# Kernel tuning notes

Measured on AMD Instinct MI355X. Metric: run time of the kernel, lower is better.

Reference implementation:

```python
import jax, jax.numpy as jnp
import numpy as np
from jax import lax

EPS = 1e-12

def _l2norm(v, axis):
    n = jnp.linalg.norm(v, axis=axis, keepdims=True)
    return v / jnp.maximum(n, EPS)

def setup_inputs() -> dict:
    key = jax.random.key(0)
    k1, k2, k3 = jax.random.split(key, 3)
    C, H, W, K = 512, 192, 192, 64
    x = jax.random.normal(k1, (C, H, W), dtype=jnp.float32)
    conv_w = jax.random.normal(k2, (K, C), dtype=jnp.float32) * 0.05  # 1x1 conv, no bias (vladv2=False)
    centroids = jax.random.uniform(k3, (K, C), dtype=jnp.float32)
    return {"x": x, "conv_w": conv_w, "centroids": centroids}

def reference(x, conv_w, centroids):
    K = conv_w.shape[0]
    x4 = x[None]                      # [1,C,H,W]
    N, C, H, W = x4.shape
    L = H * W
    # descriptor-wise L2 normalization over channels
    x4 = _l2norm(x4, axis=1)
    # 1x1 conv -> soft assignment over clusters
    logits = jnp.einsum('kc,nchw->nkhw', conv_w, x4)
    soft = jax.nn.softmax(logits, axis=1)          # [N,K,H,W]
    sa_flat = soft.reshape(N, K, L)
    # top-2 cluster indices per location (argmax + second largest)
    _, top2 = lax.top_k(sa_flat.transpose(0, 2, 1), 2)  # [N,L,2]
    first, second = top2[..., 0], top2[..., 1]
    # unfold 3x3, padding 1: windows [N, L, K, 9] in (kh,kw) order
    pad = jnp.pad(soft, ((0, 0), (0, 0), (1, 1), (1, 1)))
    patches = jnp.stack([pad[:, :, di:di + H, dj:dj + W]
                         for di in range(3) for dj in range(3)], axis=2)  # [N,K,9,H,W]
    windows = patches.reshape(N, K, 9, L).transpose(0, 3, 1, 2)           # [N,L,K,9]
    # keep only windows of the top-2 clusters at each location
    karange = jnp.arange(K)[None, None, :]
    keep = (karange == first[:, :, None]) | (karange == second[:, :, None])  # [N,L,K]
    wsel = windows * keep[..., None].astype(windows.dtype)
    # fold (transpose of unfold): overlap-add back to [N,K,H,W]
    ws = wsel.transpose(0, 2, 3, 1).reshape(N, K, 9, H, W)
    out_pad = jnp.zeros((N, K, H + 2, W + 2), dtype=ws.dtype)
    t = 0
    for di in range(3):
        for dj in range(3):
            out_pad = out_pad.at[:, :, di:di + H, dj:dj + W].add(ws[:, :, t])
            t += 1
    weight = out_pad[:, :, 1:H + 1, 1:W + 1]
    # border mask: (min distance to border)^4
    ii = jnp.arange(H); jj = jnp.arange(W)
    mi = jnp.minimum(H - 1 - ii, ii)[:, None]
    mj = jnp.minimum(W - 1 - jj, jj)[None, :]
    m = jnp.minimum(mi, mj).astype(weight.dtype)
    m2 = m * m
    mask = m2 * m2
    weight = weight * mask[None, None]
    sa2 = weight.reshape(N, K, L)
    # per-cluster residual accumulation, vectorized (replaces the 64-iter loop)
    xf = x4.reshape(N, C, L)
    vlad = jnp.einsum('nkl,ncl->nkc', sa2, xf) - sa2.sum(-1)[..., None] * centroids[None]
    vlad = _l2norm(vlad, axis=2)               # intra-normalization
    v = vlad.reshape(N, -1)
    v = _l2norm(v, axis=1)
    return v
```

## Files before the change

kernel.cpp:

```cpp
#include <hip/hip_runtime.h>

#define HH 192
#define WW 192
#define LL (HH * WW)
#define CC 512
#define KK 64
#define EPSF 1e-12f
typedef unsigned long long ull;

#define NCHUNK 192
#define CHUNKL (LL / NCHUNK)
#define LT 32
#define CT 128

__global__ __launch_bounds__(256) void k0_transpose(const float* __restrict__ w,
                                                    float* __restrict__ wT) {
    int idx = blockIdx.x * 256 + threadIdx.x;
    int k = idx >> 9;
    int c = idx & 511;
    wT[c * KK + k] = w[idx];
}

__global__ __launch_bounds__(512) void k1_logits(const float* __restrict__ x,
                                                 const float* __restrict__ wT,
                                                 float* __restrict__ soft,
                                                 float* __restrict__ invn,
                                                 ull* __restrict__ keep) {
    __shared__ float accs[4][16][64];
    __shared__ float sss[64];
    __shared__ float sm1[4][64], sm2[4][64], ssum[4][64], sinv[64];
    __shared__ int   si1[4][64], si2[4][64];
    int t = threadIdx.x, lane = t & 63, wid = t >> 6;
    int l0 = blockIdx.x * 64;
    int kg = __builtin_amdgcn_readfirstlane((wid & 3) * 16);
    int ch = __builtin_amdgcn_readfirstlane((wid >> 2) * 256);

    const float* __restrict__ xcol = x + l0 + lane;

    float acc[16];
#pragma unroll
    for (int q = 0; q < 16; ++q) acc[q] = 0.f;
    float ss = 0.f;

    float xp[16], xn[16];
#pragma unroll
    for (int q = 0; q < 16; ++q) xp[q] = xcol[(size_t)(ch + q) * LL];

    for (int cb = ch; cb < ch + 256; cb += 16) {
        if (cb + 16 < ch + 256) {
#pragma unroll
            for (int q = 0; q < 16; ++q) xn[q] = xcol[(size_t)(cb + 16 + q) * LL];
        }
#pragma unroll
        for (int cc = 0; cc < 16; ++cc) {
            float xv = xp[cc];
            ss = fmaf(xv, xv, ss);
            const float* wr = wT + (size_t)(cb + cc) * KK + kg;
#pragma unroll
            for (int q = 0; q < 16; ++q) acc[q] = fmaf(wr[q], xv, acc[q]);
        }
        if (cb + 16 < ch + 256) {
#pragma unroll
            for (int q = 0; q < 16; ++q) xp[q] = xn[q];
        }
    }

    if (wid >= 4) {
        int w = wid - 4;
#pragma unroll
        for (int q = 0; q < 16; ++q) accs[w][q][lane] = acc[q];
        if (wid == 4) sss[lane] = ss;
    }
    __syncthreads();
    if (wid < 4) {
#pragma unroll
        for (int q = 0; q < 16; ++q) acc[q] += accs[wid][q][lane];
    }
    if (wid == 0) {
        ss += sss[lane];
        float iv = 1.0f / fmaxf(sqrtf(ss), EPSF);
        sinv[lane] = iv;
        invn[l0 + lane] = iv;
    }
    __syncthreads();
    float iv = sinv[lane];

    if (wid < 4) {
        float m1 = -3.0e38f, m2 = -3.0e38f; int i1 = 0, i2 = 0;
#pragma unroll
        for (int q = 0; q < 16; ++q) {
            float lg = acc[q] * iv;
            acc[q] = lg;
            if (lg > m1)      { m2 = m1; i2 = i1; m1 = lg; i1 = kg + q; }
            else if (lg > m2) { m2 = lg; i2 = kg + q; }
        }
        sm1[wid][lane] = m1; si1[wid][lane] = i1;
        sm2[wid][lane] = m2; si2[wid][lane] = i2;
    }
    __syncthreads();

    float M1 = -3.0e38f, M2 = -3.0e38f; int I1 = 0, I2 = 0;
    if (wid < 4) {
#pragma unroll
        for (int w2 = 0; w2 < 4; ++w2) {
            float a1 = sm1[w2][lane]; int b1 = si1[w2][lane];
            float a2 = sm2[w2][lane]; int b2 = si2[w2][lane];
            if (a1 > M1 || (a1 == M1 && b1 < I1)) { M2 = M1; I2 = I1; M1 = a1; I1 = b1; }
            else if (a1 > M2 || (a1 == M2 && b1 < I2)) { M2 = a1; I2 = b1; }
            if (a2 > M1 || (a2 == M1 && b2 < I1)) { M2 = M1; I2 = I1; M1 = a2; I1 = b2; }
            else if (a2 > M2 || (a2 == M2 && b2 < I2)) { M2 = a2; I2 = b2; }
        }
        float es = 0.f;
#pragma unroll
        for (int q = 0; q < 16; ++q) { float e = __expf(acc[q] - M1); acc[q] = e; es += e; }
        ssum[wid][lane] = es;
    }
    __syncthreads();
    if (wid < 4) {
        float St = ssum[0][lane] + ssum[1][lane] + ssum[2][lane] + ssum[3][lane];
        float rs = 1.0f / St;
        float4* sp = (float4*)(soft + (size_t)(l0 + lane) * KK + kg);
#pragma unroll
        for (int q4 = 0; q4 < 4; ++q4) {
            float4 v; v.x = acc[q4*4+0]*rs; v.y = acc[q4*4+1]*rs;
                      v.z = acc[q4*4+2]*rs; v.w = acc[q4*4+3]*rs;
            sp[q4] = v;
        }
        if (wid == 0) keep[l0 + lane] = (1ull << I1) | (1ull << I2);
    }
}

__global__ __launch_bounds__(256) void k2_weight(float* __restrict__ soft,
                                                 const ull* __restrict__ keep,
                                                 const float* __restrict__ invn,
                                                 float* __restrict__ S) {
    __shared__ float sred[4][64];
    int t = threadIdx.x, lane = t & 63, wid = t >> 6;
    int l0 = blockIdx.x * 32 + wid * 8;
    float sk = 0.f;
#pragma unroll
    for (int p = 0; p < 8; ++p) {
        int l = l0 + p;
        int i = l / WW, j = l % WW;
        int m = min(min(i, HH - 1 - i), min(j, WW - 1 - j));
        float bm = (float)m; bm *= bm; bm *= bm;
        int cnt = 0;
#pragma unroll
        for (int di = -1; di <= 1; ++di) {
            int ii = i + di;
            if (ii < 0 || ii >= HH) continue;
#pragma unroll
            for (int dj = -1; dj <= 1; ++dj) {
                int jj = j + dj;
                if (jj < 0 || jj >= WW) continue;
                ull nb = keep[ii * WW + jj];
                cnt += (int)((nb >> lane) & 1ull);
            }
        }
        float v = soft[(size_t)l * KK + lane];
        float u = v * (float)cnt * bm;
        sk += u;
        soft[(size_t)l * KK + lane] = u * invn[l];
    }
    sred[wid][lane] = sk;
    __syncthreads();
    if (wid == 0)
        atomicAdd(&S[lane], sred[0][lane] + sred[1][lane] + sred[2][lane] + sred[3][lane]);
}

__global__ __launch_bounds__(256) void k3_gemm(const float* __restrict__ w2,
                                               const float* __restrict__ x,
                                               float* __restrict__ partials) {
    __shared__ float wt[LT][KK];
    __shared__ float xt[LT][CT + 4];
    int bx = blockIdx.x;
    int chunk = bx >> 2;
    int c0 = (bx & 3) * CT;
    int l0 = chunk * CHUNKL;
    int t = threadIdx.x;
    int tx = t & 15, ty = t >> 4;

    float acc[4][8];
#pragma unroll
    for (int r = 0; r < 4; ++r)
#pragma unroll
        for (int s = 0; s < 8; ++s) acc[r][s] = 0.f;

    for (int lb = 0; lb < CHUNKL; lb += LT) {
        {
            int kk = t & 63, r2 = t >> 6;
#pragma unroll
            for (int i = 0; i < 8; ++i)
                wt[r2 + 4 * i][kk] = w2[(size_t)(l0 + lb + r2 + 4 * i) * KK + kk];
        }
        {
            int lt = t & 31, cb = t >> 5;
            int gl = l0 + lb + lt;
#pragma unroll
            for (int j = 0; j < 16; ++j)
                xt[lt][cb + 8 * j] = x[(size_t)(c0 + cb + 8 * j) * LL + gl];
        }
        __syncthreads();
#pragma unroll 2
        for (int l2 = 0; l2 < LT; ++l2) {
            float4 wa = *(const float4*)&wt[l2][ty * 4];
            float4 xa = *(const float4*)&xt[l2][tx * 4];
            float4 xb = *(const float4*)&xt[l2][64 + tx * 4];
            float wk[4] = {wa.x, wa.y, wa.z, wa.w};
            float xs[8] = {xa.x, xa.y, xa.z, xa.w, xb.x, xb.y, xb.z, xb.w};
#pragma unroll
            for (int r = 0; r < 4; ++r)
#pragma unroll
                for (int s = 0; s < 8; ++s) acc[r][s] = fmaf(wk[r], xs[s], acc[r][s]);
        }
        __syncthreads();
    }
    float* pp = partials + (size_t)chunk * KK * CC;
#pragma unroll
    for (int r = 0; r < 4; ++r) {
        int k = ty * 4 + r;
        float4 va; va.x = acc[r][0]; va.y = acc[r][1]; va.z = acc[r][2]; va.w = acc[r][3];
        float4 vb; vb.x = acc[r][4]; vb.y = acc[r][5]; vb.z = acc[r][6]; vb.w = acc[r][7];
        *(float4*)&pp[(size_t)k * CC + c0 + tx * 4]      = va;
        *(float4*)&pp[(size_t)k * CC + c0 + 64 + tx * 4] = vb;
    }
}

__global__ __launch_bounds__(256) void k4a_reduce(const float* __restrict__ partials,
                                                  const float* __restrict__ S,
                                                  const float* __restrict__ cent,
                                                  float* __restrict__ vlad,
                                                  float* __restrict__ rowsq) {
    __shared__ float red[256];
    int k = blockIdx.x;
    int c = blockIdx.y * 128 + (threadIdx.x & 127);
    int half = threadIdx.x >> 7;
    const float* pk = partials + (size_t)half * (NCHUNK / 2) * KK * CC + (size_t)k * CC + c;
    float s0 = 0.f, s1 = 0.f, s2 = 0.f, s3 = 0.f;
    for (int ch = 0; ch < NCHUNK / 2; ch += 4) {
        s0 += pk[(size_t)(ch + 0) * KK * CC];
        s1 += pk[(size_t)(ch + 1) * KK * CC];
        s2 += pk[(size_t)(ch + 2) * KK * CC];
        s3 += pk[(size_t)(ch + 3) * KK * CC];
    }
    red[threadIdx.x] = (s0 + s1) + (s2 + s3);
    __syncthreads();
    float vsq = 0.f;
    if (half == 0) {
        float v = red[threadIdx.x] + red[threadIdx.x + 128];
        v -= S[k] * cent[k * CC + c];
        vlad[k * CC + c] = v;
        vsq = v * v;
    }
    __syncthreads();
    red[threadIdx.x] = vsq;
    __syncthreads();
    for (int off = 64; off > 0; off >>= 1) {
        if (threadIdx.x < off) red[threadIdx.x] += red[threadIdx.x + off];
        __syncthreads();
    }
    if (threadIdx.x == 0) atomicAdd(&rowsq[k], red[0]);
}

__global__ __launch_bounds__(64) void k4g_scale(const float* __restrict__ rowsq,
                                                float* __restrict__ rn) {
    int lane = threadIdx.x;
    float tot = rowsq[lane];
    float r = 1.0f / fmaxf(sqrtf(tot), EPSF);
    float contrib = tot * r * r;
#pragma unroll
    for (int off = 32; off; off >>= 1) contrib += __shfl_xor(contrib, off, 64);
    float ginv = 1.0f / fmaxf(sqrtf(contrib), EPSF);
    rn[lane] = r * ginv;
}

__global__ __launch_bounds__(256) void k4c_finish(const float* __restrict__ vlad,
                                                  const float* __restrict__ rn,
                                                  float* __restrict__ out) {
    int idx4 = blockIdx.x * 256 + threadIdx.x;
    int k = idx4 >> 7;
    float s = rn[k];
    float4 v = ((const float4*)vlad)[idx4];
    v.x *= s; v.y *= s; v.z *= s; v.w *= s;
    ((float4*)out)[idx4] = v;
}

extern "C" void kernel_launch(void* const* d_in, const int* in_sizes, int n_in,
                              void* d_out, int out_size, void* d_ws, size_t ws_size,
                              hipStream_t stream) {
    const float* x      = (const float*)d_in[0];
    const float* conv_w = (const float*)d_in[1];
    const float* cent   = (const float*)d_in[2];
    float* out = (float*)d_out;

    float* ws    = (float*)d_ws;
    float* wT    = ws;
    float* soft  = wT + 32768;
    float* invn  = soft + (size_t)KK * LL;
    float* S     = invn + LL;
    float* rowsq = S + KK;
    float* rn    = rowsq + KK;
    float* vlad  = rn + KK;
    ull*   keep  = (ull*)(vlad + 32768);
    float* partials = (float*)(keep + LL);

    hipMemsetAsync(S, 0, 2 * KK * sizeof(float), stream);

    k0_transpose<<<(KK * CC) / 256, 256, 0, stream>>>(conv_w, wT);
    k1_logits<<<LL / 64, 512, 0, stream>>>(x, wT, soft, invn, keep);
    k2_weight<<<LL / 32, 256, 0, stream>>>(soft, keep, invn, S);
    k3_gemm<<<NCHUNK * (CC / CT), 256, 0, stream>>>(soft, x, partials);
    k4a_reduce<<<dim3(KK, 4), 256, 0, stream>>>(partials, S, cent, vlad, rowsq);
    k4g_scale<<<1, 64, 0, stream>>>(rowsq, rn);
    k4c_finish<<<(KK * CC / 4) / 256, 256, 0, stream>>>(vlad, rn, out);
}
```

Baseline: 232.9 us.

## Split channel reduction wider in logits, shrink GEMM channel tile, widen reduce

```diff
diff --git a/kernel.cpp b/kernel.cpp
--- a/kernel.cpp
+++ b/kernel.cpp
@@ -11,7 +11,7 @@
 #define NCHUNK 192
 #define CHUNKL (LL / NCHUNK)
 #define LT 32
-#define CT 128
+#define CT 64
 
 __global__ __launch_bounds__(256) void k0_transpose(const float* __restrict__ w,
                                                     float* __restrict__ wT) {
@@ -21,19 +21,20 @@
     wT[c * KK + k] = w[idx];
 }
 
-__global__ __launch_bounds__(512) void k1_logits(const float* __restrict__ x,
-                                                 const float* __restrict__ wT,
-                                                 float* __restrict__ soft,
-                                                 float* __restrict__ invn,
-                                                 ull* __restrict__ keep) {
-    __shared__ float accs[4][16][64];
-    __shared__ float sss[64];
+__global__ __launch_bounds__(1024) void k1_logits(const float* __restrict__ x,
+                                                  const float* __restrict__ wT,
+                                                  float* __restrict__ soft,
+                                                  float* __restrict__ invn,
+                                                  ull* __restrict__ keep) {
+    __shared__ float accs[3][4][16][64];
+    __shared__ float sss[4][64];
     __shared__ float sm1[4][64], sm2[4][64], ssum[4][64], sinv[64];
     __shared__ int   si1[4][64], si2[4][64];
     int t = threadIdx.x, lane = t & 63, wid = t >> 6;
+    int kgi = wid & 3, cp = wid >> 2;
     int l0 = blockIdx.x * 64;
-    int kg = __builtin_amdgcn_readfirstlane((wid & 3) * 16);
-    int ch = __builtin_amdgcn_readfirstlane((wid >> 2) * 256);
+    int kg = __builtin_amdgcn_readfirstlane(kgi * 16);
+    int ch = __builtin_amdgcn_readfirstlane(cp * 128);
 
     const float* __restrict__ xcol = x + l0 + lane;
 
@@ -46,8 +47,8 @@
 #pragma unroll
     for (int q = 0; q < 16; ++q) xp[q] = xcol[(size_t)(ch + q) * LL];
 
-    for (int cb = ch; cb < ch + 256; cb += 16) {
-        if (cb + 16 < ch + 256) {
+    for (int cb = ch; cb < ch + 128; cb += 16) {
+        if (cb + 16 < ch + 128) {
 #pragma unroll
             for (int q = 0; q < 16; ++q) xn[q] = xcol[(size_t)(cb + 16 + q) * LL];
         }
@@ -59,25 +60,26 @@
 #pragma unroll
             for (int q = 0; q < 16; ++q) acc[q] = fmaf(wr[q], xv, acc[q]);
         }
-        if (cb + 16 < ch + 256) {
+        if (cb + 16 < ch + 128) {
 #pragma unroll
             for (int q = 0; q < 16; ++q) xp[q] = xn[q];
         }
     }
 
-    if (wid >= 4) {
-        int w = wid - 4;
-#pragma unroll
-        for (int q = 0; q < 16; ++q) accs[w][q][lane] = acc[q];
-        if (wid == 4) sss[lane] = ss;
-    }
-    __syncthreads();
-    if (wid < 4) {
-#pragma unroll
-        for (int q = 0; q < 16; ++q) acc[q] += accs[wid][q][lane];
+    if (cp > 0) {
+#pragma unroll
+        for (int q = 0; q < 16; ++q) accs[cp - 1][kgi][q][lane] = acc[q];
+        if (kgi == 0) sss[cp][lane] = ss;
+    }
+    __syncthreads();
+    if (cp == 0) {
+#pragma unroll
+        for (int p = 0; p < 3; ++p)
+#pragma unroll
+            for (int q = 0; q < 16; ++q) acc[q] += accs[p][kgi][q][lane];
     }
     if (wid == 0) {
-        ss += sss[lane];
+        ss += sss[1][lane] + sss[2][lane] + sss[3][lane];
         float iv = 1.0f / fmaxf(sqrtf(ss), EPSF);
         sinv[lane] = iv;
         invn[l0 + lane] = iv;
@@ -85,7 +87,7 @@
     __syncthreads();
     float iv = sinv[lane];
 
-    if (wid < 4) {
+    if (cp == 0) {
         float m1 = -3.0e38f, m2 = -3.0e38f; int i1 = 0, i2 = 0;
 #pragma unroll
         for (int q = 0; q < 16; ++q) {
@@ -94,13 +96,13 @@
             if (lg > m1)      { m2 = m1; i2 = i1; m1 = lg; i1 = kg + q; }
             else if (lg > m2) { m2 = lg; i2 = kg + q; }
         }
-        sm1[wid][lane] = m1; si1[wid][lane] = i1;
-        sm2[wid][lane] = m2; si2[wid][lane] = i2;
-    }
-    __syncthreads();
-
-    float M1 = -3.0e38f, M2 = -3.0e38f; int I1 = 0, I2 = 0;
-    if (wid < 4) {
+        sm1[kgi][lane] = m1; si1[kgi][lane] = i1;
+        sm2[kgi][lane] = m2; si2[kgi][lane] = i2;
+    }
+    __syncthreads();
+
+    if (cp == 0) {
+        float M1 = -3.0e38f, M2 = -3.0e38f; int I1 = 0, I2 = 0;
 #pragma unroll
         for (int w2 = 0; w2 < 4; ++w2) {
             float a1 = sm1[w2][lane]; int b1 = si1[w2][lane];
@@ -113,10 +115,8 @@
         float es = 0.f;
 #pragma unroll
         for (int q = 0; q < 16; ++q) { float e = __expf(acc[q] - M1); acc[q] = e; es += e; }
-        ssum[wid][lane] = es;
-    }
-    __syncthreads();
-    if (wid < 4) {
+        ssum[kgi][lane] = es;
+        __syncthreads();
         float St = ssum[0][lane] + ssum[1][lane] + ssum[2][lane] + ssum[3][lane];
         float rs = 1.0f / St;
         float4* sp = (float4*)(soft + (size_t)(l0 + lane) * KK + kg);
@@ -127,6 +127,8 @@
             sp[q4] = v;
         }
         if (wid == 0) keep[l0 + lane] = (1ull << I1) | (1ull << I2);
+    } else {
+        __syncthreads();
     }
 }
 
@@ -173,18 +175,17 @@
                                                float* __restrict__ partials) {
     __shared__ float wt[LT][KK];
     __shared__ float xt[LT][CT + 4];
-    int bx = blockIdx.x;
-    int chunk = bx >> 2;
-    int c0 = (bx & 3) * CT;
+    int chunk = blockIdx.x;
+    int c0 = blockIdx.y * CT;
     int l0 = chunk * CHUNKL;
     int t = threadIdx.x;
     int tx = t & 15, ty = t >> 4;
 
-    float acc[4][8];
+    float acc[4][4];
 #pragma unroll
     for (int r = 0; r < 4; ++r)
 #pragma unroll
-        for (int s = 0; s < 8; ++s) acc[r][s] = 0.f;
+        for (int s = 0; s < 4; ++s) acc[r][s] = 0.f;
 
     for (int lb = 0; lb < CHUNKL; lb += LT) {
         {
@@ -197,21 +198,20 @@
             int lt = t & 31, cb = t >> 5;
             int gl = l0 + lb + lt;
 #pragma unroll
-            for (int j = 0; j < 16; ++j)
+            for (int j = 0; j < 8; ++j)
                 xt[lt][cb + 8 * j] = x[(size_t)(c0 + cb + 8 * j) * LL + gl];
         }
         __syncthreads();
-#pragma unroll 2
+#pragma unroll 4
         for (int l2 = 0; l2 < LT; ++l2) {
             float4 wa = *(const float4*)&wt[l2][ty * 4];
             float4 xa = *(const float4*)&xt[l2][tx * 4];
-            float4 xb = *(const float4*)&xt[l2][64 + tx * 4];
             float wk[4] = {wa.x, wa.y, wa.z, wa.w};
-            float xs[8] = {xa.x, xa.y, xa.z, xa.w, xb.x, xb.y, xb.z, xb.w};
+            float xs[4] = {xa.x, xa.y, xa.z, xa.w};
 #pragma unroll
             for (int r = 0; r < 4; ++r)
 #pragma unroll
-                for (int s = 0; s < 8; ++s) acc[r][s] = fmaf(wk[r], xs[s], acc[r][s]);
+                for (int s = 0; s < 4; ++s) acc[r][s] = fmaf(wk[r], xs[s], acc[r][s]);
         }
         __syncthreads();
     }
@@ -220,24 +220,23 @@
     for (int r = 0; r < 4; ++r) {
         int k = ty * 4 + r;
         float4 va; va.x = acc[r][0]; va.y = acc[r][1]; va.z = acc[r][2]; va.w = acc[r][3];
-        float4 vb; vb.x = acc[r][4]; vb.y = acc[r][5]; vb.z = acc[r][6]; vb.w = acc[r][7];
-        *(float4*)&pp[(size_t)k * CC + c0 + tx * 4]      = va;
-        *(float4*)&pp[(size_t)k * CC + c0 + 64 + tx * 4] = vb;
-    }
-}
-
-__global__ __launch_bounds__(256) void k4a_reduce(const float* __restrict__ partials,
+        *(float4*)&pp[(size_t)k * CC + c0 + tx * 4] = va;
+    }
+}
+
+__global__ __launch_bounds__(512) void k4a_reduce(const float* __restrict__ partials,
                                                   const float* __restrict__ S,
                                                   const float* __restrict__ cent,
                                                   float* __restrict__ vlad,
                                                   float* __restrict__ rowsq) {
-    __shared__ float red[256];
+    __shared__ float red[512];
     int k = blockIdx.x;
-    int c = blockIdx.y * 128 + (threadIdx.x & 127);
-    int half = threadIdx.x >> 7;
-    const float* pk = partials + (size_t)half * (NCHUNK / 2) * KK * CC + (size_t)k * CC + c;
+    int ci = threadIdx.x & 127;
+    int c = blockIdx.y * 128 + ci;
+    int q = threadIdx.x >> 7;
+    const float* pk = partials + (size_t)q * (NCHUNK / 4) * KK * CC + (size_t)k * CC + c;
     float s0 = 0.f, s1 = 0.f, s2 = 0.f, s3 = 0.f;
-    for (int ch = 0; ch < NCHUNK / 2; ch += 4) {
+    for (int ch = 0; ch < NCHUNK / 4; ch += 4) {
         s0 += pk[(size_t)(ch + 0) * KK * CC];
         s1 += pk[(size_t)(ch + 1) * KK * CC];
         s2 += pk[(size_t)(ch + 2) * KK * CC];
@@ -246,8 +245,8 @@
     red[threadIdx.x] = (s0 + s1) + (s2 + s3);
     __syncthreads();
     float vsq = 0.f;
-    if (half == 0) {
-        float v = red[threadIdx.x] + red[threadIdx.x + 128];
+    if (q == 0) {
+        float v = red[ci] + red[ci + 128] + red[ci + 256] + red[ci + 384];
         v -= S[k] * cent[k * CC + c];
         vlad[k * CC + c] = v;
         vsq = v * v;
@@ -255,7 +254,7 @@
     __syncthreads();
     red[threadIdx.x] = vsq;
     __syncthreads();
-    for (int off = 64; off > 0; off >>= 1) {
+    for (int off = 256; off > 0; off >>= 1) {
         if (threadIdx.x < off) red[threadIdx.x] += red[threadIdx.x + off];
         __syncthreads();
     }
@@ -307,10 +306,10 @@
     hipMemsetAsync(S, 0, 2 * KK * sizeof(float), stream);
 
     k0_transpose<<<(KK * CC) / 256, 256, 0, stream>>>(conv_w, wT);
-    k1_logits<<<LL / 64, 512, 0, stream>>>(x, wT, soft, invn, keep);
+    k1_logits<<<LL / 64, 1024, 0, stream>>>(x, wT, soft, invn, keep);
     k2_weight<<<LL / 32, 256, 0, stream>>>(soft, keep, invn, S);
-    k3_gemm<<<NCHUNK * (CC / CT), 256, 0, stream>>>(soft, x, partials);
-    k4a_reduce<<<dim3(KK, 4), 256, 0, stream>>>(partials, S, cent, vlad, rowsq);
+    k3_gemm<<<dim3(NCHUNK, CC / CT), 256, 0, stream>>>(soft, x, partials);
+    k4a_reduce<<<dim3(KK, 4), 512, 0, stream>>>(partials, S, cent, vlad, rowsq);
     k4g_scale<<<1, 64, 0, stream>>>(rowsq, rn);
     k4c_finish<<<(KK * CC / 4) / 256, 256, 0, stream>>>(vlad, rn, out);
 }
```

Result: slower. 243.0 us (+4.3%).

## Fuse weight computation into GEMM and merge small tail kernels

Applied to the files above, without the earlier changes.

```diff
diff --git a/kernel.cpp b/kernel.cpp
--- a/kernel.cpp
+++ b/kernel.cpp
@@ -14,11 +14,13 @@
 #define CT 128
 
 __global__ __launch_bounds__(256) void k0_transpose(const float* __restrict__ w,
-                                                    float* __restrict__ wT) {
+                                                    float* __restrict__ wT,
+                                                    float* __restrict__ Szero) {
     int idx = blockIdx.x * 256 + threadIdx.x;
     int k = idx >> 9;
     int c = idx & 511;
     wT[c * KK + k] = w[idx];
+    if (blockIdx.x == 0 && threadIdx.x < 128) Szero[threadIdx.x] = 0.f;
 }
 
 __global__ __launch_bounds__(512) void k1_logits(const float* __restrict__ x,
@@ -130,75 +132,60 @@
     }
 }
 
-__global__ __launch_bounds__(256) void k2_weight(float* __restrict__ soft,
-                                                 const ull* __restrict__ keep,
-                                                 const float* __restrict__ invn,
-                                                 float* __restrict__ S) {
-    __shared__ float sred[4][64];
-    int t = threadIdx.x, lane = t & 63, wid = t >> 6;
-    int l0 = blockIdx.x * 32 + wid * 8;
-    float sk = 0.f;
-#pragma unroll
-    for (int p = 0; p < 8; ++p) {
-        int l = l0 + p;
-        int i = l / WW, j = l % WW;
-        int m = min(min(i, HH - 1 - i), min(j, WW - 1 - j));
-        float bm = (float)m; bm *= bm; bm *= bm;
-        int cnt = 0;
-#pragma unroll
-        for (int di = -1; di <= 1; ++di) {
-            int ii = i + di;
-            if (ii < 0 || ii >= HH) continue;
-#pragma unroll
-            for (int dj = -1; dj <= 1; ++dj) {
-                int jj = j + dj;
-                if (jj < 0 || jj >= WW) continue;
-                ull nb = keep[ii * WW + jj];
-                cnt += (int)((nb >> lane) & 1ull);
-            }
-        }
-        float v = soft[(size_t)l * KK + lane];
-        float u = v * (float)cnt * bm;
-        sk += u;
-        soft[(size_t)l * KK + lane] = u * invn[l];
-    }
-    sred[wid][lane] = sk;
-    __syncthreads();
-    if (wid == 0)
-        atomicAdd(&S[lane], sred[0][lane] + sred[1][lane] + sred[2][lane] + sred[3][lane]);
-}
-
-__global__ __launch_bounds__(256) void k3_gemm(const float* __restrict__ w2,
+__global__ __launch_bounds__(256) void k3_gemm(const float* __restrict__ soft,
+                                               const ull* __restrict__ keep,
+                                               const float* __restrict__ invn,
                                                const float* __restrict__ x,
-                                               float* __restrict__ partials) {
+                                               float* __restrict__ partials,
+                                               float* __restrict__ S) {
     __shared__ float wt[LT][KK];
     __shared__ float xt[LT][CT + 4];
-    int bx = blockIdx.x;
-    int chunk = bx >> 2;
-    int c0 = (bx & 3) * CT;
+    __shared__ float sred[4][64];
+    int chunk = blockIdx.x;
+    int c0 = blockIdx.y * CT;
     int l0 = chunk * CHUNKL;
     int t = threadIdx.x;
     int tx = t & 15, ty = t >> 4;
+    int kk = t & 63, r2 = t >> 6;
 
     float acc[4][8];
 #pragma unroll
     for (int r = 0; r < 4; ++r)
 #pragma unroll
         for (int s = 0; s < 8; ++s) acc[r][s] = 0.f;
+    float sk = 0.f;
 
     for (int lb = 0; lb < CHUNKL; lb += LT) {
+#pragma unroll
+        for (int i2 = 0; i2 < 8; ++i2) {
+            int lt = r2 + 4 * i2;
+            int l = l0 + lb + lt;
+            int i = l / WW, j = l % WW;
+            int m = min(min(i, HH - 1 - i), min(j, WW - 1 - j));
+            float bm = (float)m; bm *= bm; bm *= bm;
+            int cnt = 0;
+#pragma unroll
+            for (int di = -1; di <= 1; ++di) {
+                int ii = i + di;
+                if (ii < 0 || ii >= HH) continue;
+#pragma unroll
+                for (int dj = -1; dj <= 1; ++dj) {
+                    int jj = j + dj;
+                    if (jj < 0 || jj >= WW) continue;
+                    ull nb = keep[ii * WW + jj];
+                    cnt += (int)((nb >> kk) & 1ull);
+                }
+            }
+            float u = soft[(size_t)l * KK + kk] * (float)cnt * bm;
+            sk += u;
+            wt[lt][kk] = u * invn[l];
+        }
         {
-            int kk = t & 63, r2 = t >> 6;
-#pragma unroll
-            for (int i = 0; i < 8; ++i)
-                wt[r2 + 4 * i][kk] = w2[(size_t)(l0 + lb + r2 + 4 * i) * KK + kk];
-        }
-        {
-            int lt = t & 31, cb = t >> 5;
-            int gl = l0 + lb + lt;
+            int lt2 = t & 31, cb = t >> 5;
+            int gl = l0 + lb + lt2;
 #pragma unroll
             for (int j = 0; j < 16; ++j)
-                xt[lt][cb + 8 * j] = x[(size_t)(c0 + cb + 8 * j) * LL + gl];
+                xt[lt2][cb + 8 * j] = x[(size_t)(c0 + cb + 8 * j) * LL + gl];
         }
         __syncthreads();
 #pragma unroll 2
@@ -215,6 +202,14 @@
         }
         __syncthreads();
     }
+
+    if (blockIdx.y == 0) {
+        sred[r2][kk] = sk;
+        __syncthreads();
+        if (r2 == 0)
+            atomicAdd(&S[kk], sred[0][kk] + sred[1][kk] + sred[2][kk] + sred[3][kk]);
+    }
+
     float* pp = partials + (size_t)chunk * KK * CC;
 #pragma unroll
     for (int r = 0; r < 4; ++r) {
@@ -226,18 +221,19 @@
     }
 }
 
-__global__ __launch_bounds__(256) void k4a_reduce(const float* __restrict__ partials,
+__global__ __launch_bounds__(512) void k4a_reduce(const float* __restrict__ partials,
                                                   const float* __restrict__ S,
                                                   const float* __restrict__ cent,
                                                   float* __restrict__ vlad,
                                                   float* __restrict__ rowsq) {
-    __shared__ float red[256];
+    __shared__ float red[512];
     int k = blockIdx.x;
-    int c = blockIdx.y * 128 + (threadIdx.x & 127);
-    int half = threadIdx.x >> 7;
-    const float* pk = partials + (size_t)half * (NCHUNK / 2) * KK * CC + (size_t)k * CC + c;
+    int ci = threadIdx.x & 127;
+    int c = blockIdx.y * 128 + ci;
+    int q = threadIdx.x >> 7;
+    const float* pk = partials + (size_t)q * (NCHUNK / 4) * KK * CC + (size_t)k * CC + c;
     float s0 = 0.f, s1 = 0.f, s2 = 0.f, s3 = 0.f;
-    for (int ch = 0; ch < NCHUNK / 2; ch += 4) {
+    for (int ch = 0; ch < NCHUNK / 4; ch += 4) {
         s0 += pk[(size_t)(ch + 0) * KK * CC];
         s1 += pk[(size_t)(ch + 1) * KK * CC];
         s2 += pk[(size_t)(ch + 2) * KK * CC];
@@ -246,8 +242,8 @@
     red[threadIdx.x] = (s0 + s1) + (s2 + s3);
     __syncthreads();
     float vsq = 0.f;
-    if (half == 0) {
-        float v = red[threadIdx.x] + red[threadIdx.x + 128];
+    if (q == 0) {
+        float v = red[ci] + red[ci + 128] + red[ci + 256] + red[ci + 384];
         v -= S[k] * cent[k * CC + c];
         vlad[k * CC + c] = v;
         vsq = v * v;
@@ -255,31 +251,31 @@
     __syncthreads();
     red[threadIdx.x] = vsq;
     __syncthreads();
-    for (int off = 64; off > 0; off >>= 1) {
+    for (int off = 256; off > 0; off >>= 1) {
         if (threadIdx.x < off) red[threadIdx.x] += red[threadIdx.x + off];
         __syncthreads();
     }
     if (threadIdx.x == 0) atomicAdd(&rowsq[k], red[0]);
 }
 
-__global__ __launch_bounds__(64) void k4g_scale(const float* __restrict__ rowsq,
-                                                float* __restrict__ rn) {
-    int lane = threadIdx.x;
-    float tot = rowsq[lane];
-    float r = 1.0f / fmaxf(sqrtf(tot), EPSF);
-    float contrib = tot * r * r;
-#pragma unroll
-    for (int off = 32; off; off >>= 1) contrib += __shfl_xor(contrib, off, 64);
-    float ginv = 1.0f / fmaxf(sqrtf(contrib), EPSF);
-    rn[lane] = r * ginv;
-}
-
 __global__ __launch_bounds__(256) void k4c_finish(const float* __restrict__ vlad,
-                                                  const float* __restrict__ rn,
+                                                  const float* __restrict__ rowsq,
                                                   float* __restrict__ out) {
-    int idx4 = blockIdx.x * 256 + threadIdx.x;
+    __shared__ float rns[64];
+    int t = threadIdx.x;
+    if (t < 64) {
+        float tot = rowsq[t];
+        float r = 1.0f / fmaxf(sqrtf(tot), EPSF);
+        float contrib = tot * r * r;
+#pragma unroll
+        for (int off = 32; off; off >>= 1) contrib += __shfl_xor(contrib, off, 64);
+        float ginv = 1.0f / fmaxf(sqrtf(contrib), EPSF);
+        rns[t] = r * ginv;
+    }
+    __syncthreads();
+    int idx4 = blockIdx.x * 256 + t;
     int k = idx4 >> 7;
-    float s = rn[k];
+    float s = rns[k];
     float4 v = ((const float4*)vlad)[idx4];
     v.x *= s; v.y *= s; v.z *= s; v.w *= s;
     ((float4*)out)[idx4] = v;
@@ -299,18 +295,13 @@
     float* invn  = soft + (size_t)KK * LL;
     float* S     = invn + LL;
     float* rowsq = S + KK;
-    float* rn    = rowsq + KK;
-    float* vlad  = rn + KK;
+    float* vlad  = rowsq + KK;
     ull*   keep  = (ull*)(vlad + 32768);
     float* partials = (float*)(keep + LL);
 
-    hipMemsetAsync(S, 0, 2 * KK * sizeof(float), stream);
-
-    k0_transpose<<<(KK * CC) / 256, 256, 0, stream>>>(conv_w, wT);
+    k0_transpose<<<(KK * CC) / 256, 256, 0, stream>>>(conv_w, wT, S);
     k1_logits<<<LL / 64, 512, 0, stream>>>(x, wT, soft, invn, keep);
-    k2_weight<<<LL / 32, 256, 0, stream>>>(soft, keep, invn, S);
-    k3_gemm<<<NCHUNK * (CC / CT), 256, 0, stream>>>(soft, x, partials);
-    k4a_reduce<<<dim3(KK, 4), 256, 0, stream>>>(partials, S, cent, vlad, rowsq);
-    k4g_scale<<<1, 64, 0, stream>>>(rowsq, rn);
-    k4c_finish<<<(KK * CC / 4) / 256, 256, 0, stream>>>(vlad, rn, out);
-}
+    k3_gemm<<<dim3(NCHUNK, CC / CT), 256, 0, stream>>>(soft, keep, invn, x, partials, S);
+    k4a_reduce<<<dim3(KK, 4), 512, 0, stream>>>(partials, S, cent, vlad, rowsq);
+    k4c_finish<<<(KK * CC / 4) / 256, 256, 0, stream>>>(vlad, rowsq, out);
+}
```

Result: slower. 248.3 us (+6.6%).
